# Optimization experiments

Hardware: AMD Instinct MI355X
Metric: run time of the kernel (lower is better)

The kernel has to match this reference:

```python
import jax, jax.numpy as jnp
import numpy as np

MAX_VALUATION = 5  # init kwarg
N = 4096           # == n_samples, so subsampling branch is skipped
D = 512
IDX_MAX = 200000


def setup_inputs() -> dict:
    key = jax.random.key(0)
    k1, k2 = jax.random.split(key)
    z = jax.random.normal(k1, (N, D), dtype=jnp.float32)
    indices = jax.random.randint(k2, (N,), 0, IDX_MAX, dtype=jnp.int64 if jax.config.jax_enable_x64 else jnp.int32)
    return {"z": z, "indices": indices}


def _pairwise_dist(z):
    # torch.cdist(z, z), p=2, with a sqrt-safe formulation
    sq = jnp.sum(z * z, axis=-1)                      # [n]
    d2 = sq[:, None] + sq[None, :] - 2.0 * (z @ z.T)  # [n, n]
    d2 = jnp.maximum(d2, 0.0)
    pos = d2 > 0.0
    return jnp.where(pos, jnp.sqrt(jnp.where(pos, d2, 1.0)), 0.0)


def _valuation_capped(diff, cap):
    # v3(diff) capped at `cap`: v >= t  <=>  diff % 3**t == 0 (for diff > 0)
    val = jnp.zeros(diff.shape, dtype=jnp.int32)
    for t in range(1, cap + 1):
        val = val + (diff % (3 ** t) == 0).astype(jnp.int32)
    return val


def reference(z, indices):
    n = z.shape[0]
    dist = _pairwise_dist(z)                               # [n, n]
    diff = jnp.abs(indices[:, None] - indices[None, :])    # [n, n] int
    # cap valuation at MAX_VALUATION+1 so over-cap pairs match no level v<=MAX_VALUATION
    val = _valuation_capped(diff, MAX_VALUATION + 1)
    upper = jnp.triu(jnp.ones((n, n), dtype=bool), k=1)
    valid = upper & (diff > 0)

    total = jnp.float32(0.0)
    level_count = jnp.float32(0.0)
    for v in range(MAX_VALUATION + 1):
        target = jnp.float32(3.0 ** (-v))
        weight = jnp.float32(1.0 / (v + 1))
        mask = valid & (val == v)
        cnt = jnp.sum(mask)
        sq = jnp.where(mask, (dist - target) ** 2, 0.0)
        mse = jnp.sum(sq) / jnp.maximum(cnt, 1).astype(jnp.float32)
        use = cnt >= 2  # original skips levels with <2 pairs
        total = total + jnp.where(use, weight * mse, 0.0)
        level_count = level_count + use.astype(jnp.float32)
    return total / jnp.maximum(level_count, 1.0)
```

## Files before the change

kernel.cpp:

```cpp
#include <hip/hip_runtime.h>
#include <hip/hip_bf16.h>
#include <stdint.h>

typedef unsigned short u16;
typedef unsigned int   u32;
typedef unsigned long long u64;

#define N_ROWS 4096
#define DIM    512
#define NT64   64
#define NPAIR64 2080
#define MOD3   729
#define NLEV   6
#define NKS    16
#define NSLOT  64

typedef __attribute__((ext_vector_type(4))) float f32x4;

#define WS_ZPK 0
#define WS_SQ  (N_ROWS * DIM)
#define WS_R   (WS_SQ + N_ROWS * 4)
#define WS_ACC (WS_R + N_ROWS * 4)

__global__ __launch_bounds__(256)
void prep_kernel(const float* __restrict__ z, const int* __restrict__ idx,
                 u64* __restrict__ zpack, float* __restrict__ sq,
                 int* __restrict__ rres, u32* __restrict__ acczero)
{
    const int lane = threadIdx.x & 63;
    const int row  = blockIdx.x * 4 + (threadIdx.x >> 6);
    const float4* zr = reinterpret_cast<const float4*>(z + (size_t)row * DIM) + lane * 2;
    float4 v0 = zr[0], v1 = zr[1];
    float f[8] = {v0.x, v0.y, v0.z, v0.w, v1.x, v1.y, v1.z, v1.w};
    float ss = 0.f;
#pragma unroll
    for (int k = 0; k < 8; ++k) ss += f[k] * f[k];
    int lo = __builtin_amdgcn_cvt_pk_fp8_f32(f[0], f[1], 0, false);
    lo     = __builtin_amdgcn_cvt_pk_fp8_f32(f[2], f[3], lo, true);
    int hi = __builtin_amdgcn_cvt_pk_fp8_f32(f[4], f[5], 0, false);
    hi     = __builtin_amdgcn_cvt_pk_fp8_f32(f[6], f[7], hi, true);
    const u64 pk = (u64)(u32)lo | ((u64)(u32)hi << 32);
    zpack[((size_t)((row >> 4) * 16 + (lane >> 2)) << 6)
          + (lane & 3) * 16 + (row & 15)] = pk;
#pragma unroll
    for (int off = 32; off > 0; off >>= 1) ss += __shfl_down(ss, off, 64);
    if (lane == 0) {
        sq[row]   = ss;
        rres[row] = idx[row] % MOD3;
    }
    if (row == 0) {
#pragma unroll
        for (int i = 0; i < 16; ++i) acczero[lane + i * 64] = 0u;
    }
}

template<bool DIAG>
__device__ __forceinline__ void epilogue_acc(
    const f32x4 (&acc)[4][4], const float* sqI, const float* sqJ,
    const int* rI, const int* rJ, int lane,
    float (&lsum)[NLEV], u64& pcnt)
{
    const int rbase = (lane >> 4) * 4;
    const int cbase = lane & 15;
#pragma unroll
    for (int m = 0; m < 4; ++m) {
        const int il0 = m * 16 + rbase;
#pragma unroll
        for (int n = 0; n < 4; ++n) {
            const int jl  = n * 16 + cbase;
            const float sqj = sqJ[jl];
            const int   rj  = rJ[jl];
#pragma unroll
            for (int q = 0; q < 4; ++q) {
                const int il = il0 + q;
                float d2 = fmaxf(sqI[il] + sqj - 2.0f * acc[m][n][q], 0.f);
                const float dist = __builtin_amdgcn_sqrtf(d2);
                int dm = rI[il] - rj;
                dm += (dm >> 31) & MOD3;
                const u32 x = (u32)dm;
                int v =
                    (x * 2863311531u <= 1431655765u) +
                    (x *  954437177u <=  477218588u) +
                    (x * 1749801491u <=  159072862u) +
                    (x * 2014922929u <=   53024287u) +
                    (x * 3534952507u <=   17674762u) +
                    (x * 4041629033u <=    5891587u);
                if (DIAG) {
                    v = (jl > il) ? v : 6;
                }
                float tv = 1.0f;
                tv = (v == 1) ? (1.f / 3.f)   : tv;
                tv = (v == 2) ? (1.f / 9.f)   : tv;
                tv = (v == 3) ? (1.f / 27.f)  : tv;
                tv = (v == 4) ? (1.f / 81.f)  : tv;
                tv = (v == 5) ? (1.f / 243.f) : tv;
                const float dd  = dist - tv;
                const float sqd = dd * dd;
#pragma unroll
                for (int vv = 0; vv < NLEV; ++vv)
                    lsum[vv] += (v == vv) ? sqd : 0.f;
                pcnt += 1ull << (8 * v);
            }
        }
    }
}

__global__ __launch_bounds__(64, 2)
void pair_kernel(const u64* __restrict__ zpack, const float* __restrict__ sq,
                 const int* __restrict__ rres, float* __restrict__ gsum2,
                 u32* __restrict__ gcnt2)
{
    __shared__ __align__(16) float sqI[64];
    __shared__ __align__(16) float sqJ[64];
    __shared__ __align__(16) int   rI[64];
    __shared__ __align__(16) int   rJ[64];

    const int lane = threadIdx.x;

    const int wg = (blockIdx.x & 7) * (NPAIR64 / 8) + (blockIdx.x >> 3);
    int t = wg, ti = 0, rem = NT64;
    while (t >= rem) { t -= rem; ++ti; --rem; }
    const int tj = ti + t;
    const int I0 = ti * 64, J0 = tj * 64;

    __builtin_amdgcn_global_load_lds(
        (const __attribute__((address_space(1))) u32*)(sq + I0 + lane),
        (__attribute__((address_space(3))) u32*)sqI, 4, 0, 0);
    __builtin_amdgcn_global_load_lds(
        (const __attribute__((address_space(1))) u32*)(sq + J0 + lane),
        (__attribute__((address_space(3))) u32*)sqJ, 4, 0, 0);
    __builtin_amdgcn_global_load_lds(
        (const __attribute__((address_space(1))) u32*)(rres + I0 + lane),
        (__attribute__((address_space(3))) u32*)rI, 4, 0, 0);
    __builtin_amdgcn_global_load_lds(
        (const __attribute__((address_space(1))) u32*)(rres + J0 + lane),
        (__attribute__((address_space(3))) u32*)rJ, 4, 0, 0);

    const int RA = ti * 4;
    const int RB = tj * 4;

    f32x4 acc[4][4];
#pragma unroll
    for (int m = 0; m < 4; ++m)
#pragma unroll
        for (int n = 0; n < 4; ++n) acc[m][n] = (f32x4){0.f, 0.f, 0.f, 0.f};

    long A[8][4], B[8][4];

#define LOADF(d, s)                                                            \
    {                                                                          \
        _Pragma("unroll")                                                      \
        for (int m = 0; m < 4; ++m) {                                          \
            A[d][m] = (long)zpack[((size_t)((RA + m) * 16 + (s)) << 6) + lane];\
            B[d][m] = (long)zpack[((size_t)((RB + m) * 16 + (s)) << 6) + lane];\
        }                                                                      \
    }
#define MFMA_ALL(d)                                                            \
    {                                                                          \
        _Pragma("unroll")                                                      \
        for (int m = 0; m < 4; ++m)                                            \
            _Pragma("unroll")                                                  \
            for (int n = 0; n < 4; ++n)                                        \
                acc[m][n] = __builtin_amdgcn_mfma_f32_16x16x32_fp8_fp8(        \
                    A[d][m], B[d][n], acc[m][n], 0, 0, 0);                     \
    }

#pragma unroll
    for (int s = 0; s < 7; ++s) LOADF(s, s);
#pragma unroll
    for (int s = 0; s < NKS; ++s) {
        if (s + 7 < NKS) LOADF((s + 7) & 7, s + 7);
        MFMA_ALL(s & 7);
    }
#undef LOADF
#undef MFMA_ALL

    __builtin_amdgcn_s_waitcnt(0);

    float lsum[NLEV] = {0.f, 0.f, 0.f, 0.f, 0.f, 0.f};
    u64 pcnt = 0ull;
    if (ti == tj) epilogue_acc<true >(acc, sqI, sqJ, rI, rJ, lane, lsum, pcnt);
    else          epilogue_acc<false>(acc, sqI, sqJ, rI, rJ, lane, lsum, pcnt);

    const int slot = (int)(blockIdx.x & (NSLOT - 1));
#pragma unroll
    for (int vv = 0; vv < NLEV; ++vv) {
        float s = lsum[vv];
        u32   c = (u32)((pcnt >> (8 * vv)) & 255ull);
#pragma unroll
        for (int off = 32; off > 0; off >>= 1) {
            s += __shfl_xor(s, off, 64);
            c += __shfl_xor(c, off, 64);
        }
        if (lane == 0) {
            atomicAdd(&gsum2[slot * 8 + vv], s);
            atomicAdd(&gcnt2[slot * 8 + vv], c);
        }
    }
}

__global__ __launch_bounds__(64)
void finalize_kernel(const float* __restrict__ gsum2,
                     const u32* __restrict__ gcnt2,
                     float* __restrict__ out)
{
    const int lane = threadIdx.x;
    float s[NLEV];
    u32   c[NLEV];
#pragma unroll
    for (int v = 0; v < NLEV; ++v) {
        s[v] = gsum2[lane * 8 + v];
        c[v] = gcnt2[lane * 8 + v];
    }
#pragma unroll
    for (int v = 0; v < NLEV; ++v) {
#pragma unroll
        for (int off = 32; off > 0; off >>= 1) {
            s[v] += __shfl_xor(s[v], off, 64);
            c[v] += __shfl_xor(c[v], off, 64);
        }
    }
    if (lane == 0) {
        const float w[NLEV] = {1.f, 1.f / 2.f, 1.f / 3.f, 1.f / 4.f, 1.f / 5.f, 1.f / 6.f};
        float total = 0.f, lc = 0.f;
#pragma unroll
        for (int v = 0; v < NLEV; ++v) {
            const float cnt = (float)c[v];
            const float mse = s[v] / fmaxf(cnt, 1.f);
            const bool  use = c[v] >= 2u;
            total += use ? w[v] * mse : 0.f;
            lc    += use ? 1.f : 0.f;
        }
        out[0] = total / fmaxf(lc, 1.f);
    }
}

extern "C" void kernel_launch(void* const* d_in, const int* in_sizes, int n_in,
                              void* d_out, int out_size, void* d_ws, size_t ws_size,
                              hipStream_t stream)
{
    const float* z   = (const float*)d_in[0];
    const int*   idx = (const int*)d_in[1];
    char* ws = (char*)d_ws;
    u64*   zpk  = (u64*)(ws + WS_ZPK);
    float* sq   = (float*)(ws + WS_SQ);
    int*   rres = (int*)(ws + WS_R);
    float* gsum2 = (float*)(ws + WS_ACC);
    u32*   gcnt2 = (u32*)(ws + WS_ACC + NSLOT * 8 * 4);
    float* out  = (float*)d_out;

    prep_kernel<<<N_ROWS / 4, 256, 0, stream>>>(z, idx, zpk, sq, rres, (u32*)gsum2);
    pair_kernel<<<NPAIR64, 64, 0, stream>>>(zpk, sq, rres, gsum2, gcnt2);
    finalize_kernel<<<1, 64, 0, stream>>>(gsum2, gcnt2, out);
}
```

Baseline: 42.07 us.

## Stage fp8 operand tiles through LDS with double-buffered direct global-to-LDS loads

Reorders the packed fp8 layout so each lane holds two consecutive k-slices as a 16-byte pair. Operand tiles are then streamed into a double-buffered LDS array with 16-byte global_load_lds, and read back as long2 vectors. This replaces the old 7-deep register prefetch of 8-byte global loads. The aim is fewer, wider memory requests and lower VGPR pressure, at the cost of LDS traffic and explicit vmcnt waits, which are fragile if the compiler reorders or counts loads differently.

```diff
diff --git a/kernel.cpp b/kernel.cpp
--- a/kernel.cpp
+++ b/kernel.cpp
@@ -12,9 +12,10 @@
 #define NPAIR64 2080
 #define MOD3   729
 #define NLEV   6
-#define NKS    16
+#define NKP    8
 #define NSLOT  64
 
+typedef __attribute__((ext_vector_type(2))) long  long2v;
 typedef __attribute__((ext_vector_type(4))) float f32x4;
 
 #define WS_ZPK 0
@@ -40,8 +41,8 @@
     int hi = __builtin_amdgcn_cvt_pk_fp8_f32(f[4], f[5], 0, false);
     hi     = __builtin_amdgcn_cvt_pk_fp8_f32(f[6], f[7], hi, true);
     const u64 pk = (u64)(u32)lo | ((u64)(u32)hi << 32);
-    zpack[((size_t)((row >> 4) * 16 + (lane >> 2)) << 6)
-          + (lane & 3) * 16 + (row & 15)] = pk;
+    zpack[((size_t)((row >> 4) * 8 + (lane >> 3)) << 7)
+          + ((lane & 3) * 16 + (row & 15)) * 2 + ((lane >> 2) & 1)] = pk;
 #pragma unroll
     for (int off = 32; off > 0; off >>= 1) ss += __shfl_down(ss, off, 64);
     if (lane == 0) {
@@ -110,10 +111,9 @@
                  const int* __restrict__ rres, float* __restrict__ gsum2,
                  u32* __restrict__ gcnt2)
 {
-    __shared__ __align__(16) float sqI[64];
-    __shared__ __align__(16) float sqJ[64];
-    __shared__ __align__(16) int   rI[64];
-    __shared__ __align__(16) int   rJ[64];
+    __shared__ __align__(16) u64 sb[2][8][128];
+    __shared__ float sqI[64], sqJ[64];
+    __shared__ int   rI[64], rJ[64];
 
     const int lane = threadIdx.x;
 
@@ -136,46 +136,58 @@
         (const __attribute__((address_space(1))) u32*)(rres + J0 + lane),
         (__attribute__((address_space(3))) u32*)rJ, 4, 0, 0);
 
-    const int RA = ti * 4;
-    const int RB = tj * 4;
-
-    f32x4 acc[4][4];
-#pragma unroll
-    for (int m = 0; m < 4; ++m)
-#pragma unroll
-        for (int n = 0; n < 4; ++n) acc[m][n] = (f32x4){0.f, 0.f, 0.f, 0.f};
-
-    long A[8][4], B[8][4];
-
-#define LOADF(d, s)                                                            \
+    const int RA = ti * 4, RB = tj * 4;
+
+#define STAGE(buf, kp)                                                         \
     {                                                                          \
         _Pragma("unroll")                                                      \
-        for (int m = 0; m < 4; ++m) {                                          \
-            A[d][m] = (long)zpack[((size_t)((RA + m) * 16 + (s)) << 6) + lane];\
-            B[d][m] = (long)zpack[((size_t)((RB + m) * 16 + (s)) << 6) + lane];\
+        for (int g = 0; g < 4; ++g) {                                          \
+            __builtin_amdgcn_global_load_lds(                                  \
+                (const __attribute__((address_space(1))) u32*)                 \
+                    (zpack + (((size_t)(RA + g) * 8 + (kp)) << 7) + lane * 2), \
+                (__attribute__((address_space(3))) u32*)&sb[buf][g][0],        \
+                16, 0, 0);                                                     \
+            __builtin_amdgcn_global_load_lds(                                  \
+                (const __attribute__((address_space(1))) u32*)                 \
+                    (zpack + (((size_t)(RB + g) * 8 + (kp)) << 7) + lane * 2), \
+                (__attribute__((address_space(3))) u32*)&sb[buf][4 + g][0],    \
+                16, 0, 0);                                                     \
         }                                                                      \
     }
-#define MFMA_ALL(d)                                                            \
-    {                                                                          \
-        _Pragma("unroll")                                                      \
-        for (int m = 0; m < 4; ++m)                                            \
-            _Pragma("unroll")                                                  \
-            for (int n = 0; n < 4; ++n)                                        \
-                acc[m][n] = __builtin_amdgcn_mfma_f32_16x16x32_fp8_fp8(        \
-                    A[d][m], B[d][n], acc[m][n], 0, 0, 0);                     \
-    }
-
-#pragma unroll
-    for (int s = 0; s < 7; ++s) LOADF(s, s);
-#pragma unroll
-    for (int s = 0; s < NKS; ++s) {
-        if (s + 7 < NKS) LOADF((s + 7) & 7, s + 7);
-        MFMA_ALL(s & 7);
-    }
-#undef LOADF
-#undef MFMA_ALL
-
-    __builtin_amdgcn_s_waitcnt(0);
+
+    f32x4 acc[4][4];
+#pragma unroll
+    for (int m = 0; m < 4; ++m)
+#pragma unroll
+        for (int n = 0; n < 4; ++n) acc[m][n] = (f32x4){0.f, 0.f, 0.f, 0.f};
+
+    STAGE(0, 0);
+#pragma unroll
+    for (int kp = 0; kp < NKP; ++kp) {
+        const int buf = kp & 1;
+        if (kp + 1 < NKP) {
+            STAGE(buf ^ 1, kp + 1);
+            asm volatile("s_waitcnt vmcnt(8)" ::: "memory");
+        } else {
+            asm volatile("s_waitcnt vmcnt(0)" ::: "memory");
+        }
+        __builtin_amdgcn_sched_barrier(0);
+        long2v A[4], B[4];
+#pragma unroll
+        for (int g = 0; g < 4; ++g) {
+            A[g] = reinterpret_cast<const long2v*>(&sb[buf][g][0])[lane];
+            B[g] = reinterpret_cast<const long2v*>(&sb[buf][4 + g][0])[lane];
+        }
+#pragma unroll
+        for (int h = 0; h < 2; ++h)
+#pragma unroll
+            for (int m = 0; m < 4; ++m)
+#pragma unroll
+                for (int n = 0; n < 4; ++n)
+                    acc[m][n] = __builtin_amdgcn_mfma_f32_16x16x32_fp8_fp8(
+                        A[m][h], B[n][h], acc[m][n], 0, 0, 0);
+    }
+#undef STAGE
 
     float lsum[NLEV] = {0.f, 0.f, 0.f, 0.f, 0.f, 0.f};
     u64 pcnt = 0ull;
@@ -242,12 +254,12 @@
     const float* z   = (const float*)d_in[0];
     const int*   idx = (const int*)d_in[1];
     char* ws = (char*)d_ws;
-    u64*   zpk  = (u64*)(ws + WS_ZPK);
-    float* sq   = (float*)(ws + WS_SQ);
-    int*   rres = (int*)(ws + WS_R);
+    u64*   zpk   = (u64*)(ws + WS_ZPK);
+    float* sq    = (float*)(ws + WS_SQ);
+    int*   rres  = (int*)(ws + WS_R);
     float* gsum2 = (float*)(ws + WS_ACC);
     u32*   gcnt2 = (u32*)(ws + WS_ACC + NSLOT * 8 * 4);
-    float* out  = (float*)d_out;
+    float* out   = (float*)d_out;
 
     prep_kernel<<<N_ROWS / 4, 256, 0, stream>>>(z, idx, zpk, sq, rres, (u32*)gsum2);
     pair_kernel<<<NPAIR64, 64, 0, stream>>>(zpk, sq, rres, gsum2, gcnt2);
```

Result: faster. 37.39 us (-11.1%).
